# Performance work log

Measured on AMD Instinct MI355X. Metric: run time of the kernel, lower is better.

The kernel has to match this reference:

```python
import jax, jax.numpy as jnp
import numpy as np

N = 50000
E = 800000
IN_DIM = 128
HID = 64
HEADS = 4
OUT_DIM = 121
NEG_SLOPE = 0.2
EPS = 1e-16


def setup_inputs() -> dict:
    key = jax.random.key(0)
    ks = jax.random.split(key, 16)
    glorot = lambda k, shape: jax.random.normal(k, shape, jnp.float32) * (2.0 / (shape[0] + shape[-1])) ** 0.5
    HC = HEADS * HID
    return {
        "x": jax.random.normal(ks[0], (N, IN_DIM), jnp.float32),
        "edge_index": jax.random.randint(ks[1], (2, E), 0, N, jnp.int64),
        # conv1: GATConv(IN_DIM -> HID, heads=HEADS, concat)
        "W1": glorot(ks[2], (IN_DIM, HC)),
        "att_src1": glorot(ks[3], (HEADS, HID)),
        "att_dst1": glorot(ks[4], (HEADS, HID)),
        "b1": jnp.zeros((HC,), jnp.float32),
        # conv2: GATConv(HC -> HID, heads=HEADS, concat)
        "W2": glorot(ks[5], (HC, HC)),
        "att_src2": glorot(ks[6], (HEADS, HID)),
        "att_dst2": glorot(ks[7], (HEADS, HID)),
        "b2": jnp.zeros((HC,), jnp.float32),
        # post_mp: Linear(HC, HID) -> Dropout -> Linear(HID, OUT_DIM)
        "Wm1": glorot(ks[8], (HC, HID)),
        "bm1": jnp.zeros((HID,), jnp.float32),
        "Wm2": glorot(ks[9], (HID, OUT_DIM)),
        "bm2": jnp.zeros((OUT_DIM,), jnp.float32),
    }


def gat_conv(x, src, dst, W, att_src, att_dst, b):
    """PyG GATConv (concat=True, add_self_loops already applied to src/dst)."""
    n = x.shape[0]
    h = (x @ W).reshape(n, HEADS, -1)                     # [N, H, C]
    a_s = jnp.einsum("nhc,hc->nh", h, att_src)            # [N, H]
    a_d = jnp.einsum("nhc,hc->nh", h, att_dst)            # [N, H]
    e = jax.nn.leaky_relu(a_s[src] + a_d[dst], NEG_SLOPE)  # [Etot, H]
    # segment softmax over destination nodes
    m = jax.ops.segment_max(e, dst, num_segments=n)       # [N, H]
    ex = jnp.exp(e - m[dst])
    denom = jax.ops.segment_sum(ex, dst, num_segments=n)  # [N, H]
    alpha = ex / (denom[dst] + EPS)                        # [Etot, H]
    out = jax.ops.segment_sum(alpha[:, :, None] * h[src], dst, num_segments=n)  # [N, H, C]
    return out.reshape(n, -1) + b


def reference(x, edge_index, W1, att_src1, att_dst1, b1, W2, att_src2, att_dst2, b2, Wm1, bm1, Wm2, bm2):
    n = x.shape[0]
    loops = jnp.arange(n, dtype=edge_index.dtype)
    src = jnp.concatenate([edge_index[0], loops])
    dst = jnp.concatenate([edge_index[1], loops])
    h = jax.nn.relu(gat_conv(x, src, dst, W1, att_src1, att_dst1, b1))
    h = jax.nn.relu(gat_conv(h, src, dst, W2, att_src2, att_dst2, b2))
    h = h @ Wm1 + bm1
    h = h @ Wm2 + bm2
    return jax.nn.sigmoid(h)
```

## Files before the change

### kernel.cpp

```cpp
#include <hip/hip_runtime.h>
#include <hip/hip_bf16.h>
#include <float.h>

#define HEADS 4
#define HID 64
#define HC 256
#define NEG_SLOPE 0.2f
#define EPS 1e-16f
#define SLOG 7
#define SLOTS 128

typedef short bf16x8 __attribute__((ext_vector_type(8)));
typedef float f32x4 __attribute__((ext_vector_type(4)));
typedef unsigned short ushort8 __attribute__((ext_vector_type(8)));

__device__ __forceinline__ float bflo(unsigned u) { return __uint_as_float(u << 16); }
__device__ __forceinline__ float bfhi(unsigned u) { return __uint_as_float(u & 0xffff0000u); }
__device__ __forceinline__ unsigned packbf2(float a, float b) {
  __hip_bfloat16 ha = __float2bfloat16(a), hb = __float2bfloat16(b);
  unsigned short ua = *reinterpret_cast<unsigned short*>(&ha);
  unsigned short ub = *reinterpret_cast<unsigned short*>(&hb);
  return (unsigned)ua | ((unsigned)ub << 16);
}

#define PK 40

__global__ void __launch_bounds__(512) conv_gemm_attn(
    const __hip_bfloat16* __restrict__ A, const __hip_bfloat16* __restrict__ Bt,
    __hip_bfloat16* __restrict__ Cb,
    const float* __restrict__ att_s, const float* __restrict__ att_d,
    float* __restrict__ a_s, float* __restrict__ a_d,
    float* __restrict__ blockmax, int M, int K) {
  __shared__ unsigned short As[2][64 * PK];
  __shared__ unsigned short Bs[2][256 * PK];
  int tid = threadIdx.x;
  int lane = tid & 63, w = tid >> 6;
  int col16 = lane & 15, quad = lane >> 4;
  int r0 = (w >> 2) * 32;
  int c0 = (w & 3) * 64;
  int row0 = blockIdx.x * 64;
  const unsigned short* Ag = (const unsigned short*)A;
  const unsigned short* Bg = (const unsigned short*)Bt;

  bool doA = tid < 256;
  int ar = (tid & 255) >> 2;
  int ako = (tid & 3) << 3;
  int agr = row0 + ar; if (agr >= M) agr = M - 1;
  const unsigned short* aga = Ag + (size_t)agr * K + ako;

  f32x4 acc[2][4] = {};
  int niter = K >> 5;

  ushort8 pa, pb[2];
  if (doA) pa = *(const ushort8*)(aga);
#pragma unroll
  for (int p = 0; p < 2; p++) {
    int i2 = tid + (p << 9);
    int br = i2 >> 2, bko = (i2 & 3) << 3;
    pb[p] = *(const ushort8*)(Bg + (size_t)br * K + bko);
  }
  if (doA) *(ushort8*)(&As[0][ar * PK + ako]) = pa;
#pragma unroll
  for (int p = 0; p < 2; p++) {
    int i2 = tid + (p << 9);
    int br = i2 >> 2, bko = (i2 & 3) << 3;
    *(ushort8*)(&Bs[0][br * PK + bko]) = pb[p];
  }
  __syncthreads();

  for (int it = 0; it < niter; ++it) {
    int cur = it & 1, nxt = cur ^ 1;
    int k1 = (it + 1) << 5;
    if (it + 1 < niter) {
      if (doA) pa = *(const ushort8*)(aga + k1);
#pragma unroll
      for (int p = 0; p < 2; p++) {
        int i2 = tid + (p << 9);
        int br = i2 >> 2, bko = (i2 & 3) << 3;
        pb[p] = *(const ushort8*)(Bg + (size_t)br * K + k1 + bko);
      }
    }
    bf16x8 a[2], b[4];
#pragma unroll
    for (int i = 0; i < 2; i++)
      a[i] = *(const bf16x8*)(&As[cur][(r0 + i * 16 + col16) * PK + quad * 8]);
#pragma unroll
    for (int j = 0; j < 4; j++)
      b[j] = *(const bf16x8*)(&Bs[cur][(c0 + j * 16 + col16) * PK + quad * 8]);
#pragma unroll
    for (int i = 0; i < 2; i++)
#pragma unroll
      for (int j = 0; j < 4; j++)
        acc[i][j] = __builtin_amdgcn_mfma_f32_16x16x32_bf16(a[i], b[j], acc[i][j], 0, 0, 0);
    if (it + 1 < niter) {
      if (doA) *(ushort8*)(&As[nxt][ar * PK + ako]) = pa;
#pragma unroll
      for (int p = 0; p < 2; p++) {
        int i2 = tid + (p << 9);
        int br = i2 >> 2, bko = (i2 & 3) << 3;
        *(ushort8*)(&Bs[nxt][br * PK + bko]) = pb[p];
      }
    }
    __syncthreads();
  }

#pragma unroll
  for (int i = 0; i < 2; i++) {
#pragma unroll
    for (int j = 0; j < 4; j++) {
      int gc = c0 + j * 16 + col16;
      int grb = row0 + r0 + i * 16 + quad * 4;
#pragma unroll
      for (int r = 0; r < 4; r++) {
        int gr = grb + r;
        if (gr < M) Cb[(size_t)gr * 256 + gc] = __float2bfloat16(acc[i][j][r]);
      }
    }
  }

  float ws4[4], wd4[4];
#pragma unroll
  for (int j = 0; j < 4; j++) {
    ws4[j] = att_s[c0 + j * 16 + col16];
    wd4[j] = att_d[c0 + j * 16 + col16];
  }
  float wavemax = -FLT_MAX;
#pragma unroll
  for (int i = 0; i < 2; i++) {
#pragma unroll
    for (int r = 0; r < 4; r++) {
      float vs = 0.f, vd = 0.f;
#pragma unroll
      for (int j = 0; j < 4; j++) {
        vs += acc[i][j][r] * ws4[j];
        vd += acc[i][j][r] * wd4[j];
      }
#pragma unroll
      for (int off = 1; off < 16; off <<= 1) {
        vs += __shfl_xor(vs, off);
        vd += __shfl_xor(vd, off);
      }
      int gr = row0 + r0 + i * 16 + quad * 4 + r;
      if (col16 == 0 && gr < M) {
        a_s[(size_t)gr * 4 + (w & 3)] = vs;
        a_d[(size_t)gr * 4 + (w & 3)] = vd;
      }
      wavemax = fmaxf(wavemax, vs);
    }
  }
  wavemax = fmaxf(wavemax, __shfl_xor(wavemax, 16));
  wavemax = fmaxf(wavemax, __shfl_xor(wavemax, 32));
  float* wmx = (float*)&As[0][0];
  if (lane == 0) wmx[w] = wavemax;
  __syncthreads();
  if (w < 4 && lane == 0)
    blockmax[(size_t)blockIdx.x * 4 + w] = fmaxf(wmx[w], wmx[w + 4]);
}

__global__ void __launch_bounds__(256) reduce_gmax(const float* __restrict__ blockmax,
                                                   float* __restrict__ gmaxf, int goff, int nb) {
  __shared__ float wm[4][4];
  int tid = threadIdx.x, lane = tid & 63, w = tid >> 6;
  int hd = tid & 3;
  float m = -FLT_MAX;
  for (int i = tid >> 2; i < nb; i += 64)
    m = fmaxf(m, blockmax[(size_t)i * 4 + hd]);
#pragma unroll
  for (int off = 4; off < 64; off <<= 1)
    m = fmaxf(m, __shfl_xor(m, off));
  if (lane < 4) wm[w][lane] = m;
  __syncthreads();
  if (tid < 4) {
    float r = fmaxf(fmaxf(wm[0][tid], wm[1][tid]), fmaxf(wm[2][tid], wm[3][tid]));
    gmaxf[goff + tid] = r;
  }
}

#define TS 72

__global__ void __launch_bounds__(256) postmp_fused(
    const __hip_bfloat16* __restrict__ A, const __hip_bfloat16* __restrict__ Wm1t,
    const __hip_bfloat16* __restrict__ Wm2t, const float* __restrict__ bm1,
    const float* __restrict__ bm2, float* __restrict__ out, int M) {
  __shared__ unsigned short smem[24576];
  unsigned short* W2s = &smem[15360];
  int tid = threadIdx.x;
  int lane = tid & 63, w = tid >> 6;
  int col16 = lane & 15, quad = lane >> 4;
  int row0 = blockIdx.x * 128;
  const unsigned short* Ag = (const unsigned short*)A;
  const unsigned short* Bg = (const unsigned short*)Wm1t;
  const unsigned short* W2g = (const unsigned short*)Wm2t;

#pragma unroll
  for (int c = tid; c < 1024; c += 256) {
    int r = c >> 3, ko = (c & 7) << 3;
    ushort8 v = {};
    if (r < 121) v = *(const ushort8*)(W2g + (size_t)r * 64 + ko);
    *(ushort8*)(&W2s[r * TS + ko]) = v;
  }

  int ar0 = tid >> 2, ako = (tid & 3) << 3;
  int agr0 = row0 + ar0;       if (agr0 >= M) agr0 = M - 1;
  int agr1 = row0 + ar0 + 64;  if (agr1 >= M) agr1 = M - 1;
  const unsigned short* aga0 = Ag + (size_t)agr0 * 256 + ako;
  const unsigned short* aga1 = Ag + (size_t)agr1 * 256 + ako;
  int br = tid >> 2, bko = (tid & 3) << 3;
  const unsigned short* bga = Bg + (size_t)br * 256 + bko;

  f32x4 acc1[2][4] = {};
  ushort8 pa0, pa1, pbv;
  pa0 = *(const ushort8*)(aga0);
  pa1 = *(const ushort8*)(aga1);
  pbv = *(const ushort8*)(bga);
  *(ushort8*)(&smem[ar0 * PK + ako]) = pa0;
  *(ushort8*)(&smem[(ar0 + 64) * PK + ako]) = pa1;
  *(ushort8*)(&smem[10240 + br * PK + bko]) = pbv;
  __syncthreads();

  for (int it = 0; it < 8; ++it) {
    int cur = it & 1, nxt = cur ^ 1;
    unsigned short* Asc = &smem[cur * 5120];
    unsigned short* Bsc = &smem[10240 + cur * 2560];
    int k1 = (it + 1) << 5;
    if (it + 1 < 8) {
      pa0 = *(const ushort8*)(aga0 + k1);
      pa1 = *(const ushort8*)(aga1 + k1);
      pbv = *(const ushort8*)(bga + k1);
    }
    bf16x8 a[2], b[4];
#pragma unroll
    for (int i = 0; i < 2; i++)
      a[i] = *(const bf16x8*)(&Asc[(w * 32 + i * 16 + col16) * PK + quad * 8]);
#pragma unroll
    for (int j = 0; j < 4; j++)
      b[j] = *(const bf16x8*)(&Bsc[(j * 16 + col16) * PK + quad * 8]);
#pragma unroll
    for (int i = 0; i < 2; i++)
#pragma unroll
      for (int j = 0; j < 4; j++)
        acc1[i][j] = __builtin_amdgcn_mfma_f32_16x16x32_bf16(a[i], b[j], acc1[i][j], 0, 0, 0);
    if (it + 1 < 8) {
      unsigned short* Asn = &smem[nxt * 5120];
      unsigned short* Bsn = &smem[10240 + nxt * 2560];
      *(ushort8*)(&Asn[ar0 * PK + ako]) = pa0;
      *(ushort8*)(&Asn[(ar0 + 64) * PK + ako]) = pa1;
      *(ushort8*)(&Bsn[br * PK + bko]) = pbv;
    }
    __syncthreads();
  }

  unsigned short* T = &smem[0];
#pragma unroll
  for (int i = 0; i < 2; i++) {
#pragma unroll
    for (int j = 0; j < 4; j++) {
      int col = j * 16 + col16;
      float bv = bm1[col];
#pragma unroll
      for (int r = 0; r < 4; r++) {
        int rl = w * 32 + i * 16 + quad * 4 + r;
        __hip_bfloat16 hv = __float2bfloat16(acc1[i][j][r] + bv);
        T[rl * TS + col] = *reinterpret_cast<unsigned short*>(&hv);
      }
    }
  }
  __syncthreads();

  int wm2 = w & 1, wn2 = w >> 1;
  f32x4 acc2[4][4] = {};
#pragma unroll
  for (int kk = 0; kk < 2; kk++) {
    bf16x8 a[4], b[4];
#pragma unroll
    for (int i = 0; i < 4; i++)
      a[i] = *(const bf16x8*)(&T[(wm2 * 64 + i * 16 + col16) * TS + kk * 32 + quad * 8]);
#pragma unroll
    for (int j = 0; j < 4; j++)
      b[j] = *(const bf16x8*)(&W2s[(wn2 * 64 + j * 16 + col16) * TS + kk * 32 + quad * 8]);
#pragma unroll
    for (int i = 0; i < 4; i++)
#pragma unroll
      for (int j = 0; j < 4; j++)
        acc2[i][j] = __builtin_amdgcn_mfma_f32_16x16x32_bf16(a[i], b[j], acc2[i][j], 0, 0, 0);
  }
#pragma unroll
  for (int i = 0; i < 4; i++) {
#pragma unroll
    for (int j = 0; j < 4; j++) {
      int gc = wn2 * 64 + j * 16 + col16;
      if (gc >= 121) continue;
      float bv = bm2[gc];
      int grb = row0 + wm2 * 64 + i * 16 + quad * 4;
#pragma unroll
      for (int r = 0; r < 4; r++) {
        int gr = grb + r;
        if (gr >= M) continue;
        float v = acc2[i][j][r] + bv;
        out[(size_t)gr * 121 + gc] = 1.f / (1.f + __expf(-v));
      }
    }
  }
}

__global__ void setup_all(const float* __restrict__ x, __hip_bfloat16* __restrict__ xb,
                          const float* __restrict__ W1, const float* __restrict__ W2,
                          const float* __restrict__ Wm1, const float* __restrict__ Wm2,
                          __hip_bfloat16* __restrict__ W1t, __hip_bfloat16* __restrict__ W2t,
                          __hip_bfloat16* __restrict__ Wm1t, __hip_bfloat16* __restrict__ Wm2t,
                          int* __restrict__ cur, int* __restrict__ slots,
                          int n, int castBlocks, int prepBlocks) {
  int b = blockIdx.x;
  int tid = threadIdx.x;
  if (b < castBlocks) {
    int i = b * 256 + tid;
    if (i < n * 32) {
      float4 v = *(const float4*)(x + 4 * (size_t)i);
      uint2 pk;
      pk.x = packbf2(v.x, v.y);
      pk.y = packbf2(v.z, v.w);
      *(uint2*)((unsigned*)xb + 2 * (size_t)i) = pk;
    }
    return;
  }
  b -= castBlocks;
  if (b < prepBlocks) {
    int i = b * 256 + tid;
    if (i < 128 * 256) {
      int nn = i / 128, kk = i - nn * 128;
      W1t[i] = __float2bfloat16(W1[(size_t)kk * 256 + nn]);
      return;
    }
    i -= 128 * 256;
    if (i < 256 * 256) {
      int nn = i / 256, kk = i - nn * 256;
      W2t[i] = __float2bfloat16(W2[(size_t)kk * 256 + nn]);
      return;
    }
    i -= 256 * 256;
    if (i < 256 * 64) {
      int nn = i / 256, kk = i - nn * 256;
      Wm1t[i] = __float2bfloat16(Wm1[(size_t)kk * 64 + nn]);
      return;
    }
    i -= 256 * 64;
    if (i < 64 * 121) {
      int nn = i / 64, kk = i - nn * 64;
      Wm2t[i] = __float2bfloat16(Wm2[(size_t)kk * 121 + nn]);
    }
    return;
  }
  b -= prepBlocks;
  {
    int i = b * 256 + tid;
    if (i < n) {
      cur[i] = 1;
      slots[(size_t)i << SLOG] = i;
    }
  }
}

__global__ void slot_fill(const int* __restrict__ ei, int E,
                          int* __restrict__ cur, int* __restrict__ slots) {
  int i = blockIdx.x * 256 + threadIdx.x;
  if (i >= E) return;
  int s = ei[i], d = ei[E + i];
  int pos = atomicAdd(&cur[d], 1);
  slots[((size_t)d << SLOG) + pos] = s;
}

__global__ void __launch_bounds__(256) gat_aggregate(
    const __hip_bfloat16* __restrict__ hb, const float* __restrict__ a_src,
    const float* __restrict__ a_dst, const int* __restrict__ cnt_arr,
    const int* __restrict__ slots, const float* __restrict__ bias,
    const float* __restrict__ gmaxf, int goff,
    __hip_bfloat16* __restrict__ out, int n) {
  __shared__ float plds[4][256];
  int wid = threadIdx.x >> 6;
  int lane = threadIdx.x & 63;
  int half = lane >> 5;
  int l32 = lane & 31;
  int qh = l32 >> 3;
  int node = (blockIdx.x << 2) + wid;
  if (node >= n) return;
  float4 adv = *(const float4*)(a_dst + (size_t)node * 4);
  float m0 = gmaxf[goff + 0] + adv.x; m0 = fmaxf(m0, NEG_SLOPE * m0);
  float m1 = gmaxf[goff + 1] + adv.y; m1 = fmaxf(m1, NEG_SLOPE * m1);
  float m2 = gmaxf[goff + 2] + adv.z; m2 = fmaxf(m2, NEG_SLOPE * m2);
  float m3 = gmaxf[goff + 3] + adv.w; m3 = fmaxf(m3, NEG_SLOPE * m3);
  int cntN = __builtin_amdgcn_readfirstlane(cnt_arr[node]);
  int beg = node << SLOG;
  const uint4* hw4 = (const uint4*)hb;

  float lq = 0.f;
  float c0 = 0.f, c1 = 0.f, c2 = 0.f, c3 = 0.f;
  float c4 = 0.f, c5 = 0.f, c6 = 0.f, c7 = 0.f;

  for (int cbeg = 0; cbeg < cntN; cbeg += 64) {
    int cnt = cntN - cbeg; if (cnt > 64) cnt = 64;
    int eidx = beg + cbeg + (lane < cnt ? lane : cnt - 1);
    int s_l = slots[eidx];
    float4 as = *(const float4*)(a_src + (size_t)s_l * 4);
    float v0 = as.x + adv.x; v0 = fmaxf(v0, NEG_SLOPE * v0);
    float v1 = as.y + adv.y; v1 = fmaxf(v1, NEG_SLOPE * v1);
    float v2 = as.z + adv.z; v2 = fmaxf(v2, NEG_SLOPE * v2);
    float v3 = as.w + adv.w; v3 = fmaxf(v3, NEG_SLOPE * v3);
    float p0 = __expf(v0 - m0), p1 = __expf(v1 - m1);
    float p2 = __expf(v2 - m2), p3 = __expf(v3 - m3);
    *(float4*)&plds[wid][lane * 4] = make_float4(p0, p1, p2, p3);
    __builtin_amdgcn_s_waitcnt(0);

    auto step = [&](int j) {
      int jj = j + half;
      bool dup = jj >= cnt;
      int jc = dup ? cnt - 1 : jj;
      int sj = __shfl(s_l, jc);
      float pq = plds[wid][jc * 4 + qh];
      if (dup) pq = 0.f;
      uint4 d = hw4[(size_t)sj * 32 + l32];
      c0 += pq * bflo(d.x); c1 += pq * bfhi(d.x);
      c2 += pq * bflo(d.y); c3 += pq * bfhi(d.y);
      c4 += pq * bflo(d.z); c5 += pq * bfhi(d.z);
      c6 += pq * bflo(d.w); c7 += pq * bfhi(d.w);
      lq += pq;
    };
    for (int j = 0; j < cnt; j += 8) { step(j); step(j + 2); step(j + 4); step(j + 6); }
  }

  lq += __shfl_xor(lq, 32);
  c0 += __shfl_xor(c0, 32); c1 += __shfl_xor(c1, 32);
  c2 += __shfl_xor(c2, 32); c3 += __shfl_xor(c3, 32);
  c4 += __shfl_xor(c4, 32); c5 += __shfl_xor(c5, 32);
  c6 += __shfl_xor(c6, 32); c7 += __shfl_xor(c7, 32);

  if (half == 0) {
    float4 bA = *(const float4*)(bias + 8 * l32);
    float4 bB = *(const float4*)(bias + 8 * l32 + 4);
    float rq = 1.f / (lq + EPS);
    float o0 = fmaxf(c0 * rq + bA.x, 0.f);
    float o1 = fmaxf(c1 * rq + bA.y, 0.f);
    float o2 = fmaxf(c2 * rq + bA.z, 0.f);
    float o3 = fmaxf(c3 * rq + bA.w, 0.f);
    float o4 = fmaxf(c4 * rq + bB.x, 0.f);
    float o5 = fmaxf(c5 * rq + bB.y, 0.f);
    float o6 = fmaxf(c6 * rq + bB.z, 0.f);
    float o7 = fmaxf(c7 * rq + bB.w, 0.f);
    uint4 pk;
    pk.x = packbf2(o0, o1);
    pk.y = packbf2(o2, o3);
    pk.z = packbf2(o4, o5);
    pk.w = packbf2(o6, o7);
    *(uint4*)((unsigned*)out + (size_t)node * 128 + l32 * 4) = pk;
  }
}

extern "C" void kernel_launch(void* const* d_in, const int* in_sizes, int n_in,
                              void* d_out, int out_size, void* d_ws, size_t ws_size,
                              hipStream_t stream) {
  const float* x      = (const float*)d_in[0];
  const int*   ei     = (const int*)d_in[1];
  const float* W1     = (const float*)d_in[2];
  const float* att_s1 = (const float*)d_in[3];
  const float* att_d1 = (const float*)d_in[4];
  const float* b1     = (const float*)d_in[5];
  const float* W2     = (const float*)d_in[6];
  const float* att_s2 = (const float*)d_in[7];
  const float* att_d2 = (const float*)d_in[8];
  const float* b2     = (const float*)d_in[9];
  const float* Wm1    = (const float*)d_in[10];
  const float* bm1    = (const float*)d_in[11];
  const float* Wm2    = (const float*)d_in[12];
  const float* bm2    = (const float*)d_in[13];
  float* out = (float*)d_out;

  int n = in_sizes[0] / 128;
  int E = in_sizes[1] / 2;

  char* ws = (char*)d_ws;
  size_t off = 0;
  auto carve = [&](size_t bytes) {
    char* p = ws + off;
    off += (bytes + 255) & ~(size_t)255;
    return p;
  };
  __hip_bfloat16* hb   = (__hip_bfloat16*)carve((size_t)n * HC * 2);
  __hip_bfloat16* aggb = (__hip_bfloat16*)carve((size_t)n * HC * 2);
  __hip_bfloat16* xb   = (__hip_bfloat16*)carve((size_t)n * 128 * 2);
  __hip_bfloat16* W1t  = (__hip_bfloat16*)carve((size_t)128 * HC * 2);
  __hip_bfloat16* W2t  = (__hip_bfloat16*)carve((size_t)HC * HC * 2);
  __hip_bfloat16* Wm1t = (__hip_bfloat16*)carve((size_t)HC * HID * 2);
  __hip_bfloat16* Wm2t = (__hip_bfloat16*)carve((size_t)HID * 121 * 2);
  float* as    = (float*)carve((size_t)n * HEADS * 4);
  float* ad    = (float*)carve((size_t)n * HEADS * 4);
  int*   cur   = (int*)carve((size_t)n * 4);
  int*   slots = (int*)carve(((size_t)n << SLOG) * 4);
  float* blockmax = (float*)carve((size_t)((n + 63) / 64) * 4 * 4);
  float* gmaxf    = (float*)carve((size_t)8 * 4);
  (void)ws_size;

  int rows64 = (n + 63) / 64;
  int castBlocks = (n * 32 + 255) / 256;
  int prepBlocks = (122432 + 255) / 256;
  int slotBlocks = (n + 255) / 256;

  setup_all<<<castBlocks + prepBlocks + slotBlocks, 256, 0, stream>>>(
      x, xb, W1, W2, Wm1, Wm2, W1t, W2t, Wm1t, Wm2t, cur, slots,
      n, castBlocks, prepBlocks);
  slot_fill<<<(E + 255) / 256, 256, 0, stream>>>(ei, E, cur, slots);

  conv_gemm_attn<<<rows64, 512, 0, stream>>>(
      xb, W1t, hb, att_s1, att_d1, as, ad, blockmax, n, 128);
  reduce_gmax<<<1, 256, 0, stream>>>(blockmax, gmaxf, 0, rows64);
  gat_aggregate<<<(n + 3) / 4, 256, 0, stream>>>(hb, as, ad, cur, slots, b1, gmaxf, 0, aggb, n);

  conv_gemm_attn<<<rows64, 512, 0, stream>>>(
      aggb, W2t, hb, att_s2, att_d2, as, ad, blockmax, n, HC);
  reduce_gmax<<<1, 256, 0, stream>>>(blockmax, gmaxf, 4, rows64);
  gat_aggregate<<<(n + 3) / 4, 256, 0, stream>>>(hb, as, ad, cur, slots, b2, gmaxf, 4, aggb, n);

  postmp_fused<<<(n + 127) / 128, 256, 0, stream>>>(aggb, Wm1t, Wm2t, bm1, bm2, out, n);
}
```

Measured before the change: 357.4 us.

## Fuse x bf16 cast into GEMM and compute per-node softmax max in aggregate

The first GEMM now reads fp32 x directly and converts it to bf16 while loading tiles, which removes the separate cast pass and the xb buffer. The global-max softmax stabiliser, which needed per-block max writes and a single-block reduce_gmax kernel per layer, is replaced by an exact per-destination max computed with wave shuffles inside gat_aggregate. This drops two kernel launches and a serial reduction, and improves numerical behaviour. In exchange, nodes with more than 64 neighbours read their slots and a_src twice, and the GEMM reads twice as many bytes for A in layer one.

```diff
diff --git a/kernel.cpp b/kernel.cpp
--- a/kernel.cpp
+++ b/kernel.cpp
@@ -25,12 +25,12 @@
 
 #define PK 40
 
+template<bool F32A>
 __global__ void __launch_bounds__(512) conv_gemm_attn(
-    const __hip_bfloat16* __restrict__ A, const __hip_bfloat16* __restrict__ Bt,
+    const void* __restrict__ Ain, const __hip_bfloat16* __restrict__ Bt,
     __hip_bfloat16* __restrict__ Cb,
     const float* __restrict__ att_s, const float* __restrict__ att_d,
-    float* __restrict__ a_s, float* __restrict__ a_d,
-    float* __restrict__ blockmax, int M, int K) {
+    float* __restrict__ a_s, float* __restrict__ a_d, int M, int K) {
   __shared__ unsigned short As[2][64 * PK];
   __shared__ unsigned short Bs[2][256 * PK];
   int tid = threadIdx.x;
@@ -39,7 +39,8 @@
   int r0 = (w >> 2) * 32;
   int c0 = (w & 3) * 64;
   int row0 = blockIdx.x * 64;
-  const unsigned short* Ag = (const unsigned short*)A;
+  const unsigned short* Ag = (const unsigned short*)Ain;
+  const float* Af = (const float*)Ain;
   const unsigned short* Bg = (const unsigned short*)Bt;
 
   bool doA = tid < 256;
@@ -47,12 +48,30 @@
   int ako = (tid & 3) << 3;
   int agr = row0 + ar; if (agr >= M) agr = M - 1;
   const unsigned short* aga = Ag + (size_t)agr * K + ako;
+  const float* agaf = Af + (size_t)agr * K + ako;
+
+  auto loadA = [&](int koff) -> ushort8 {
+    if constexpr (F32A) {
+      float4 f0 = *(const float4*)(agaf + koff);
+      float4 f1 = *(const float4*)(agaf + koff + 4);
+      unsigned p0 = packbf2(f0.x, f0.y), p1 = packbf2(f0.z, f0.w);
+      unsigned p2 = packbf2(f1.x, f1.y), p3 = packbf2(f1.z, f1.w);
+      ushort8 r;
+      r[0] = (unsigned short)p0; r[1] = (unsigned short)(p0 >> 16);
+      r[2] = (unsigned short)p1; r[3] = (unsigned short)(p1 >> 16);
+      r[4] = (unsigned short)p2; r[5] = (unsigned short)(p2 >> 16);
+      r[6] = (unsigned short)p3; r[7] = (unsigned short)(p3 >> 16);
+      return r;
+    } else {
+      return *(const ushort8*)(aga + koff);
+    }
+  };
 
   f32x4 acc[2][4] = {};
   int niter = K >> 5;
 
   ushort8 pa, pb[2];
-  if (doA) pa = *(const ushort8*)(aga);
+  if (doA) pa = loadA(0);
 #pragma unroll
   for (int p = 0; p < 2; p++) {
     int i2 = tid + (p << 9);
@@ -72,7 +91,7 @@
     int cur = it & 1, nxt = cur ^ 1;
     int k1 = (it + 1) << 5;
     if (it + 1 < niter) {
-      if (doA) pa = *(const ushort8*)(aga + k1);
+      if (doA) pa = loadA(k1);
 #pragma unroll
       for (int p = 0; p < 2; p++) {
         int i2 = tid + (p << 9);
@@ -124,7 +143,6 @@
     ws4[j] = att_s[c0 + j * 16 + col16];
     wd4[j] = att_d[c0 + j * 16 + col16];
   }
-  float wavemax = -FLT_MAX;
 #pragma unroll
   for (int i = 0; i < 2; i++) {
 #pragma unroll
@@ -145,34 +163,7 @@
         a_s[(size_t)gr * 4 + (w & 3)] = vs;
         a_d[(size_t)gr * 4 + (w & 3)] = vd;
       }
-      wavemax = fmaxf(wavemax, vs);
-    }
-  }
-  wavemax = fmaxf(wavemax, __shfl_xor(wavemax, 16));
-  wavemax = fmaxf(wavemax, __shfl_xor(wavemax, 32));
-  float* wmx = (float*)&As[0][0];
-  if (lane == 0) wmx[w] = wavemax;
-  __syncthreads();
-  if (w < 4 && lane == 0)
-    blockmax[(size_t)blockIdx.x * 4 + w] = fmaxf(wmx[w], wmx[w + 4]);
-}
-
-__global__ void __launch_bounds__(256) reduce_gmax(const float* __restrict__ blockmax,
-                                                   float* __restrict__ gmaxf, int goff, int nb) {
-  __shared__ float wm[4][4];
-  int tid = threadIdx.x, lane = tid & 63, w = tid >> 6;
-  int hd = tid & 3;
-  float m = -FLT_MAX;
-  for (int i = tid >> 2; i < nb; i += 64)
-    m = fmaxf(m, blockmax[(size_t)i * 4 + hd]);
-#pragma unroll
-  for (int off = 4; off < 64; off <<= 1)
-    m = fmaxf(m, __shfl_xor(m, off));
-  if (lane < 4) wm[w][lane] = m;
-  __syncthreads();
-  if (tid < 4) {
-    float r = fmaxf(fmaxf(wm[0][tid], wm[1][tid]), fmaxf(wm[2][tid], wm[3][tid]));
-    gmaxf[goff + tid] = r;
+    }
   }
 }
 
@@ -303,27 +294,14 @@
   }
 }
 
-__global__ void setup_all(const float* __restrict__ x, __hip_bfloat16* __restrict__ xb,
-                          const float* __restrict__ W1, const float* __restrict__ W2,
+__global__ void setup_all(const float* __restrict__ W1, const float* __restrict__ W2,
                           const float* __restrict__ Wm1, const float* __restrict__ Wm2,
                           __hip_bfloat16* __restrict__ W1t, __hip_bfloat16* __restrict__ W2t,
                           __hip_bfloat16* __restrict__ Wm1t, __hip_bfloat16* __restrict__ Wm2t,
                           int* __restrict__ cur, int* __restrict__ slots,
-                          int n, int castBlocks, int prepBlocks) {
+                          int n, int prepBlocks) {
   int b = blockIdx.x;
   int tid = threadIdx.x;
-  if (b < castBlocks) {
-    int i = b * 256 + tid;
-    if (i < n * 32) {
-      float4 v = *(const float4*)(x + 4 * (size_t)i);
-      uint2 pk;
-      pk.x = packbf2(v.x, v.y);
-      pk.y = packbf2(v.z, v.w);
-      *(uint2*)((unsigned*)xb + 2 * (size_t)i) = pk;
-    }
-    return;
-  }
-  b -= castBlocks;
   if (b < prepBlocks) {
     int i = b * 256 + tid;
     if (i < 128 * 256) {
@@ -373,7 +351,6 @@
     const __hip_bfloat16* __restrict__ hb, const float* __restrict__ a_src,
     const float* __restrict__ a_dst, const int* __restrict__ cnt_arr,
     const int* __restrict__ slots, const float* __restrict__ bias,
-    const float* __restrict__ gmaxf, int goff,
     __hip_bfloat16* __restrict__ out, int n) {
   __shared__ float plds[4][256];
   int wid = threadIdx.x >> 6;
@@ -384,10 +361,6 @@
   int node = (blockIdx.x << 2) + wid;
   if (node >= n) return;
   float4 adv = *(const float4*)(a_dst + (size_t)node * 4);
-  float m0 = gmaxf[goff + 0] + adv.x; m0 = fmaxf(m0, NEG_SLOPE * m0);
-  float m1 = gmaxf[goff + 1] + adv.y; m1 = fmaxf(m1, NEG_SLOPE * m1);
-  float m2 = gmaxf[goff + 2] + adv.z; m2 = fmaxf(m2, NEG_SLOPE * m2);
-  float m3 = gmaxf[goff + 3] + adv.w; m3 = fmaxf(m3, NEG_SLOPE * m3);
   int cntN = __builtin_amdgcn_readfirstlane(cnt_arr[node]);
   int beg = node << SLOG;
   const uint4* hw4 = (const uint4*)hb;
@@ -396,20 +369,7 @@
   float c0 = 0.f, c1 = 0.f, c2 = 0.f, c3 = 0.f;
   float c4 = 0.f, c5 = 0.f, c6 = 0.f, c7 = 0.f;
 
-  for (int cbeg = 0; cbeg < cntN; cbeg += 64) {
-    int cnt = cntN - cbeg; if (cnt > 64) cnt = 64;
-    int eidx = beg + cbeg + (lane < cnt ? lane : cnt - 1);
-    int s_l = slots[eidx];
-    float4 as = *(const float4*)(a_src + (size_t)s_l * 4);
-    float v0 = as.x + adv.x; v0 = fmaxf(v0, NEG_SLOPE * v0);
-    float v1 = as.y + adv.y; v1 = fmaxf(v1, NEG_SLOPE * v1);
-    float v2 = as.z + adv.z; v2 = fmaxf(v2, NEG_SLOPE * v2);
-    float v3 = as.w + adv.w; v3 = fmaxf(v3, NEG_SLOPE * v3);
-    float p0 = __expf(v0 - m0), p1 = __expf(v1 - m1);
-    float p2 = __expf(v2 - m2), p3 = __expf(v3 - m3);
-    *(float4*)&plds[wid][lane * 4] = make_float4(p0, p1, p2, p3);
-    __builtin_amdgcn_s_waitcnt(0);
-
+  auto gather = [&](int s_l, int cnt) {
     auto step = [&](int j) {
       int jj = j + half;
       bool dup = jj >= cnt;
@@ -425,6 +385,65 @@
       lq += pq;
     };
     for (int j = 0; j < cnt; j += 8) { step(j); step(j + 2); step(j + 4); step(j + 6); }
+  };
+
+  if (cntN <= 64) {
+    int eidx = beg + (lane < cntN ? lane : cntN - 1);
+    int s_l = slots[eidx];
+    float4 as = *(const float4*)(a_src + (size_t)s_l * 4);
+    float v0 = as.x + adv.x; v0 = fmaxf(v0, NEG_SLOPE * v0);
+    float v1 = as.y + adv.y; v1 = fmaxf(v1, NEG_SLOPE * v1);
+    float v2 = as.z + adv.z; v2 = fmaxf(v2, NEG_SLOPE * v2);
+    float v3 = as.w + adv.w; v3 = fmaxf(v3, NEG_SLOPE * v3);
+    float m0 = v0, m1 = v1, m2 = v2, m3 = v3;
+#pragma unroll
+    for (int off = 1; off < 64; off <<= 1) {
+      m0 = fmaxf(m0, __shfl_xor(m0, off));
+      m1 = fmaxf(m1, __shfl_xor(m1, off));
+      m2 = fmaxf(m2, __shfl_xor(m2, off));
+      m3 = fmaxf(m3, __shfl_xor(m3, off));
+    }
+    float p0 = __expf(v0 - m0), p1 = __expf(v1 - m1);
+    float p2 = __expf(v2 - m2), p3 = __expf(v3 - m3);
+    *(float4*)&plds[wid][lane * 4] = make_float4(p0, p1, p2, p3);
+    __builtin_amdgcn_s_waitcnt(0);
+    gather(s_l, cntN);
+  } else {
+    float m0 = -FLT_MAX, m1 = -FLT_MAX, m2 = -FLT_MAX, m3 = -FLT_MAX;
+    for (int cbeg = 0; cbeg < cntN; cbeg += 64) {
+      int cnt = cntN - cbeg; if (cnt > 64) cnt = 64;
+      int eidx = beg + cbeg + (lane < cnt ? lane : cnt - 1);
+      int s_l = slots[eidx];
+      float4 as = *(const float4*)(a_src + (size_t)s_l * 4);
+      float v0 = as.x + adv.x; v0 = fmaxf(v0, NEG_SLOPE * v0);
+      float v1 = as.y + adv.y; v1 = fmaxf(v1, NEG_SLOPE * v1);
+      float v2 = as.z + adv.z; v2 = fmaxf(v2, NEG_SLOPE * v2);
+      float v3 = as.w + adv.w; v3 = fmaxf(v3, NEG_SLOPE * v3);
+      m0 = fmaxf(m0, v0); m1 = fmaxf(m1, v1);
+      m2 = fmaxf(m2, v2); m3 = fmaxf(m3, v3);
+    }
+#pragma unroll
+    for (int off = 1; off < 64; off <<= 1) {
+      m0 = fmaxf(m0, __shfl_xor(m0, off));
+      m1 = fmaxf(m1, __shfl_xor(m1, off));
+      m2 = fmaxf(m2, __shfl_xor(m2, off));
+      m3 = fmaxf(m3, __shfl_xor(m3, off));
+    }
+    for (int cbeg = 0; cbeg < cntN; cbeg += 64) {
+      int cnt = cntN - cbeg; if (cnt > 64) cnt = 64;
+      int eidx = beg + cbeg + (lane < cnt ? lane : cnt - 1);
+      int s_l = slots[eidx];
+      float4 as = *(const float4*)(a_src + (size_t)s_l * 4);
+      float v0 = as.x + adv.x; v0 = fmaxf(v0, NEG_SLOPE * v0);
+      float v1 = as.y + adv.y; v1 = fmaxf(v1, NEG_SLOPE * v1);
+      float v2 = as.z + adv.z; v2 = fmaxf(v2, NEG_SLOPE * v2);
+      float v3 = as.w + adv.w; v3 = fmaxf(v3, NEG_SLOPE * v3);
+      float p0 = __expf(v0 - m0), p1 = __expf(v1 - m1);
+      float p2 = __expf(v2 - m2), p3 = __expf(v3 - m3);
+      *(float4*)&plds[wid][lane * 4] = make_float4(p0, p1, p2, p3);
+      __builtin_amdgcn_s_waitcnt(0);
+      gather(s_l, cnt);
+    }
   }
 
   lq += __shfl_xor(lq, 32);
@@ -485,7 +504,6 @@
   };
   __hip_bfloat16* hb   = (__hip_bfloat16*)carve((size_t)n * HC * 2);
   __hip_bfloat16* aggb = (__hip_bfloat16*)carve((size_t)n * HC * 2);
-  __hip_bfloat16* xb   = (__hip_bfloat16*)carve((size_t)n * 128 * 2);
   __hip_bfloat16* W1t  = (__hip_bfloat16*)carve((size_t)128 * HC * 2);
   __hip_bfloat16* W2t  = (__hip_bfloat16*)carve((size_t)HC * HC * 2);
   __hip_bfloat16* Wm1t = (__hip_bfloat16*)carve((size_t)HC * HID * 2);
@@ -494,29 +512,23 @@
   float* ad    = (float*)carve((size_t)n * HEADS * 4);
   int*   cur   = (int*)carve((size_t)n * 4);
   int*   slots = (int*)carve(((size_t)n << SLOG) * 4);
-  float* blockmax = (float*)carve((size_t)((n + 63) / 64) * 4 * 4);
-  float* gmaxf    = (float*)carve((size_t)8 * 4);
   (void)ws_size;
 
   int rows64 = (n + 63) / 64;
-  int castBlocks = (n * 32 + 255) / 256;
   int prepBlocks = (122432 + 255) / 256;
   int slotBlocks = (n + 255) / 256;
 
-  setup_all<<<castBlocks + prepBlocks + slotBlocks, 256, 0, stream>>>(
-      x, xb, W1, W2, Wm1, Wm2, W1t, W2t, Wm1t, Wm2t, cur, slots,
-      n, castBlocks, prepBlocks);
+  setup_all<<<prepBlocks + slotBlocks, 256, 0, stream>>>(
+      W1, W2, Wm1, Wm2, W1t, W2t, Wm1t, Wm2t, cur, slots, n, prepBlocks);
   slot_fill<<<(E + 255) / 256, 256, 0, stream>>>(ei, E, cur, slots);
 
-  conv_gemm_attn<<<rows64, 512, 0, stream>>>(
-      xb, W1t, hb, att_s1, att_d1, as, ad, blockmax, n, 128);
-  reduce_gmax<<<1, 256, 0, stream>>>(blockmax, gmaxf, 0, rows64);
-  gat_aggregate<<<(n + 3) / 4, 256, 0, stream>>>(hb, as, ad, cur, slots, b1, gmaxf, 0, aggb, n);
-
-  conv_gemm_attn<<<rows64, 512, 0, stream>>>(
-      aggb, W2t, hb, att_s2, att_d2, as, ad, blockmax, n, HC);
-  reduce_gmax<<<1, 256, 0, stream>>>(blockmax, gmaxf, 4, rows64);
-  gat_aggregate<<<(n + 3) / 4, 256, 0, stream>>>(hb, as, ad, cur, slots, b2, gmaxf, 4, aggb, n);
+  conv_gemm_attn<true><<<rows64, 512, 0, stream>>>(
+      x, W1t, hb, att_s1, att_d1, as, ad, n, 128);
+  gat_aggregate<<<(n + 3) / 4, 256, 0, stream>>>(hb, as, ad, cur, slots, b1, aggb, n);
+
+  conv_gemm_attn<false><<<rows64, 512, 0, stream>>>(
+      aggb, W2t, hb, att_s2, att_d2, as, ad, n, HC);
+  gat_aggregate<<<(n + 3) / 4, 256, 0, stream>>>(hb, as, ad, cur, slots, b2, aggb, n);
 
   postmp_fused<<<(n + 127) / 128, 256, 0, stream>>>(aggb, Wm1t, Wm2t, bm1, bm2, out, n);
 }
```

Result: faster. 347.0 us (-2.9%).
